# Kernel optimization log

Hardware: AMD Instinct MI355X
Metric: run time of the kernel (lower is better)

Reference implementation:

```python
import jax, jax.numpy as jnp
import numpy as np

N, C, H, W = 2, 256, 128, 128
NH, P = 8, 4
DH = C // NH
PAD = 1            # int(sqrt(n_points)//2)
HP, WP = H + 2 * PAD, W + 2 * PAD
LQ = H * W
DW_KS = 7


def _grid():
    # _generate_dilation_grids with n_points=4, dilation_rates=[1]:
    # kernel_size=2, linspace(0,1,2); torch stacks [y, x] (y-first quirk preserved)
    lin = np.linspace(0.0, 1.0, 2, dtype=np.float32)
    ky, kx = np.meshgrid(lin, lin, indexing='ij')
    return jnp.asarray(np.stack([ky, kx], -1).reshape(P, 2))  # (P, 2)


def _forward(query, reference_points, dw_kernel, dw_bias, ln_w, ln_b,
             W_off, b_off, W_attn, b_attn, W_val, b_val, W_out, b_out):
    # ---- dw_conv branch: depthwise 7x7 conv + channel LayerNorm + exact GELU ----
    q_img = query.transpose(0, 2, 1).reshape(N, C, H, W)
    q_img = jax.lax.conv_general_dilated(
        q_img, dw_kernel, (1, 1), [(3, 3), (3, 3)],
        dimension_numbers=('NCHW', 'OIHW', 'NCHW'), feature_group_count=C
    ) + dw_bias[None, :, None, None]
    mu = q_img.mean(axis=1, keepdims=True)
    var = ((q_img - mu) ** 2).mean(axis=1, keepdims=True)
    q_img = (q_img - mu) * jax.lax.rsqrt(var + 1e-5) * ln_w[None, :, None, None] + ln_b[None, :, None, None]
    q_img = jax.nn.gelu(q_img, approximate=False)
    q = q_img.transpose(0, 2, 3, 1).reshape(N, LQ, C)

    # ---- value projection + zero padding around the H x W map ----
    value = q @ W_val + b_val
    value = jnp.pad(value.reshape(N, H, W, C), ((0, 0), (PAD, PAD), (PAD, PAD), (0, 0)))
    v = value.reshape(N, HP * WP, NH, DH).transpose(0, 2, 1, 3)  # (N, NH, S, DH)

    # ---- offsets, sigmoid attention weights ----
    off = (q @ W_off + b_off).reshape(N, LQ, NH, 1, P, 2)
    attn = jax.nn.sigmoid(q @ W_attn + b_attn).reshape(N, LQ, NH, P)  # n_levels=1

    grid = _grid()[None, None, None, None, :, :]               # (1,1,1,1,P,2)
    norm = jnp.array([WP, HP], dtype=query.dtype)              # (W, H) normalizer
    loc = reference_points[:, :, None, :, None, :] + (grid + off) / norm
    loc = loc[:, :, :, 0, :, :]                                # (N, LQ, NH, P, 2)

    # grid_sample bilinear, align_corners=False, zero padding
    x = loc[..., 0] * WP - 0.5
    y = loc[..., 1] * HP - 0.5
    x0 = jnp.floor(x)
    y0 = jnp.floor(y)
    wx1 = x - x0
    wx0 = 1.0 - wx1
    wy1 = y - y0
    wy0 = 1.0 - wy1
    x0i = x0.astype(jnp.int32)
    y0i = y0.astype(jnp.int32)

    def gather(xi, yi):
        valid = (xi >= 0) & (xi < WP) & (yi >= 0) & (yi < HP)
        idx = jnp.clip(yi, 0, HP - 1) * WP + jnp.clip(xi, 0, WP - 1)
        idx = idx.transpose(0, 2, 1, 3).reshape(N, NH, LQ * P)
        g = jnp.take_along_axis(v, idx[..., None], axis=2)     # (N, NH, LQ*P, DH)
        m = valid.transpose(0, 2, 1, 3).reshape(N, NH, LQ * P, 1)
        return jnp.where(m, g, 0.0)

    def wmul(w):
        return w.transpose(0, 2, 1, 3).reshape(N, NH, LQ * P, 1)

    samp = (gather(x0i, y0i) * wmul(wx0 * wy0)
            + gather(x0i + 1, y0i) * wmul(wx1 * wy0)
            + gather(x0i, y0i + 1) * wmul(wx0 * wy1)
            + gather(x0i + 1, y0i + 1) * wmul(wx1 * wy1))      # (N, NH, LQ*P, DH)

    samp = samp.reshape(N, NH, LQ, P, DH)
    aw = attn.transpose(0, 2, 1, 3)[..., None]                 # (N, NH, LQ, P, 1)
    out = (samp * aw).sum(axis=3)                              # (N, NH, LQ, DH)
    out = out.transpose(0, 2, 1, 3).reshape(N, LQ, C)
    return out @ W_out + b_out


def setup_inputs() -> dict:
    key = jax.random.key(0)
    ks = jax.random.split(key, 8)
    return dict(
        query=jax.random.normal(ks[0], (N, LQ, C), jnp.float32),
        reference_points=jax.random.uniform(ks[1], (N, LQ, 1, 2), dtype=jnp.float32),
        input_spatial_shapes=jnp.array([[HP, WP]], dtype=jnp.int32),
        input_level_start_index=jnp.zeros((1,), dtype=jnp.int32),
        dw_kernel=jax.random.normal(ks[2], (C, 1, DW_KS, DW_KS), jnp.float32) * 0.05,
        dw_bias=jnp.zeros((C,), jnp.float32),
        ln_w=jnp.ones((C,), jnp.float32),
        ln_b=jnp.zeros((C,), jnp.float32),
        W_off=jax.random.normal(ks[3], (C, NH * P * 2), jnp.float32) * 0.01,
        b_off=jnp.zeros((NH * P * 2,), jnp.float32),
        W_attn=jax.random.normal(ks[4], (C, NH * P), jnp.float32) * 0.02,
        b_attn=jnp.zeros((NH * P,), jnp.float32),
        W_val=jax.random.normal(ks[5], (C, C), jnp.float32) * (1.0 / 16.0),
        b_val=jnp.zeros((C,), jnp.float32),
        W_out=jax.random.normal(ks[6], (C, C), jnp.float32) * (1.0 / 16.0),
        b_out=jnp.zeros((C,), jnp.float32),
    )


def reference(query, reference_points, input_spatial_shapes, input_level_start_index,
              dw_kernel, dw_bias, ln_w, ln_b, W_off, b_off, W_attn, b_attn,
              W_val, b_val, W_out, b_out):
    # input_spatial_shapes / input_level_start_index are static metadata (baked into constants)
    return _forward(query, reference_points, dw_kernel, dw_bias, ln_w, ln_b,
                    W_off, b_off, W_attn, b_attn, W_val, b_val, W_out, b_out)
```

## Files before the change

kernel.cpp:

```cpp
#include <hip/hip_runtime.h>
#include <hip/hip_bf16.h>
#include <hip/hip_fp16.h>
#include <math.h>

#define NB   2
#define CC   256
#define HH   128
#define WW   128
#define HPP  130
#define WPP  130
#define LQ   16384

typedef __attribute__((ext_vector_type(8))) short short8;
typedef __attribute__((ext_vector_type(8))) unsigned short u16x8;
typedef __attribute__((ext_vector_type(4))) float f32x4;
typedef __attribute__((ext_vector_type(4))) unsigned int u32x4;

static __device__ __forceinline__ unsigned short f2bf(float f) {
    __hip_bfloat16 h = __float2bfloat16(f);
    return __builtin_bit_cast(unsigned short, h);
}
static __device__ __forceinline__ float bf2f(unsigned short u) {
    unsigned int x = ((unsigned int)u) << 16;
    return __builtin_bit_cast(float, x);
}

static __device__ __forceinline__ float gelu_fast(float x) {
    float u = x * x;
    float t = x * fmaf(0.044715f, u, 1.0f);
    float e = __builtin_amdgcn_exp2f(t * 2.3022083f);
    float r = __builtin_amdgcn_rcpf(e + 1.0f);
    return x - x * r;
}

__global__ __launch_bounds__(256) void prep_kernel(
    const float* __restrict__ dwk,
    const float* __restrict__ Wval,
    const float* __restrict__ Wout,
    const float* __restrict__ Woff, const float* __restrict__ boff,
    const float* __restrict__ Wattn, const float* __restrict__ battn,
    const float* __restrict__ query,
    __half* __restrict__ kth,
    unsigned short* __restrict__ wt_val,
    unsigned short* __restrict__ wt_out,
    unsigned short* __restrict__ wt_oa,
    float* __restrict__ b_oa,
    unsigned short* __restrict__ vpad,
    __half* __restrict__ qh)
{
    int b = blockIdx.x;
    int t = threadIdx.x;
    if (b < 49) {
        kth[b * CC + t] = __float2half(dwk[t * 49 + b]);
    } else if (b < 305) {
        int k = b - 49;
        wt_val[(size_t)t * 256 + k] = f2bf(Wval[(size_t)k * 256 + t]);
    } else if (b < 561) {
        int k = b - 305;
        wt_out[(size_t)t * 256 + k] = f2bf(Wout[(size_t)k * 256 + t]);
    } else if (b < 817) {
        int k = b - 561;
        if (t < 128) {
            float v = 0.f, bb = 0.f;
            if (t < 64)      { v = Woff[(size_t)k * 64 + t];        bb = boff[t]; }
            else if (t < 96) { v = Wattn[(size_t)k * 32 + (t - 64)]; bb = battn[t - 64]; }
            wt_oa[(size_t)t * 256 + k] = f2bf(v);
            if (k == 0) b_oa[t] = bb;
        }
    } else if (b < 1849) {
        int bb = b - 817;
        int n = (bb >= 516) ? 1 : 0;
        int i = bb - n * 516;
        int y, x;
        if (i < 130)      { y = 0;           x = i; }
        else if (i < 260) { y = 129;         x = i - 130; }
        else if (i < 388) { y = i - 260 + 1; x = 0; }
        else              { y = i - 388 + 1; x = 129; }
        vpad[(((size_t)n * HPP + y) * WPP + x) * CC + t] = 0;
    } else {
        size_t idx0 = (size_t)(b - 1849) * 2048 + (size_t)t * 8;
        const float4* src = reinterpret_cast<const float4*>(query + idx0);
        float4 f0 = src[0];
        float4 f1 = src[1];
        __half2 h0 = __floats2half2_rn(f0.x, f0.y);
        __half2 h1 = __floats2half2_rn(f0.z, f0.w);
        __half2 h2 = __floats2half2_rn(f1.x, f1.y);
        __half2 h3 = __floats2half2_rn(f1.z, f1.w);
        u32x4 o;
        o.x = __builtin_bit_cast(unsigned int, h0);
        o.y = __builtin_bit_cast(unsigned int, h1);
        o.z = __builtin_bit_cast(unsigned int, h2);
        o.w = __builtin_bit_cast(unsigned int, h3);
        *reinterpret_cast<u32x4*>(qh + idx0) = o;
    }
}

__global__ __launch_bounds__(128) void conv_ln_gelu_kernel(
    const __half* __restrict__ qh,
    const __half* __restrict__ kth,
    const float* __restrict__ kbias,
    const float* __restrict__ lnw,
    const float* __restrict__ lnb,
    unsigned short* __restrict__ qact)
{
    int t  = threadIdx.x;
    int w0 = blockIdx.x * 8;
    int h  = blockIdx.y;
    int n  = blockIdx.z;

    const __half2* qn  = reinterpret_cast<const __half2*>(qh + (size_t)n * LQ * CC) + t;
    const __half2* ktc = reinterpret_cast<const __half2*>(kth) + t;

    __half2 acc[8];
    #pragma unroll
    for (int i = 0; i < 8; ++i) acc[i] = __half2(0.f, 0.f);

    if (w0 >= 8 && w0 <= 112 && h >= 3 && h <= 124) {
        #pragma unroll
        for (int ky = 0; ky < 7; ++ky) {
            const __half2* qrow = qn + ((size_t)(h + ky - 3) * WW + (w0 - 3)) * 128;
            __half2 wt[7];
            #pragma unroll
            for (int kx = 0; kx < 7; ++kx)
                wt[kx] = ktc[(ky * 7 + kx) * 128];
            __half2 in[14];
            #pragma unroll
            for (int j = 0; j < 14; ++j)
                in[j] = qrow[(size_t)j * 128];
            #pragma unroll
            for (int i = 0; i < 8; ++i)
                #pragma unroll
                for (int kx = 0; kx < 7; ++kx)
                    acc[i] = __hfma2(in[i + kx], wt[kx], acc[i]);
        }
    } else {
        #pragma unroll
        for (int ky = 0; ky < 7; ++ky) {
            int iy = h + ky - 3;
            if (iy < 0 || iy >= HH) continue;
            const __half2* qrow = qn + (size_t)iy * WW * 128;
            __half2 wt[7];
            #pragma unroll
            for (int kx = 0; kx < 7; ++kx)
                wt[kx] = ktc[(ky * 7 + kx) * 128];
            __half2 in[14];
            #pragma unroll
            for (int j = 0; j < 14; ++j) {
                int ix = w0 - 3 + j;
                in[j] = (ix >= 0 && ix < WW) ? qrow[(size_t)ix * 128]
                                             : __half2(0.f, 0.f);
            }
            #pragma unroll
            for (int i = 0; i < 8; ++i)
                #pragma unroll
                for (int kx = 0; kx < 7; ++kx)
                    acc[i] = __hfma2(in[i + kx], wt[kx], acc[i]);
        }
    }

    float b0 = kbias[2 * t];
    float b1 = kbias[2 * t + 1];
    float a0[8], a1[8];
    #pragma unroll
    for (int i = 0; i < 8; ++i) {
        a0[i] = __low2float(acc[i])  + b0;
        a1[i] = __high2float(acc[i]) + b1;
    }

    __shared__ float lsum[8][2];
    __shared__ float lsq[8][2];
    int lane = t & 63;
    int wv   = t >> 6;

    #pragma unroll
    for (int i = 0; i < 8; ++i) {
        float s  = a0[i] + a1[i];
        float sq = a0[i] * a0[i] + a1[i] * a1[i];
        #pragma unroll
        for (int m = 1; m < 64; m <<= 1) {
            s  += __shfl_xor(s,  m);
            sq += __shfl_xor(sq, m);
        }
        if (lane == 0) { lsum[i][wv] = s; lsq[i][wv] = sq; }
    }
    __syncthreads();

    float lw0 = lnw[2 * t], lw1 = lnw[2 * t + 1];
    float lb0 = lnb[2 * t], lb1 = lnb[2 * t + 1];
    unsigned short* qo = qact + (((size_t)n * LQ) + (size_t)h * WW + w0) * CC + 2 * t;

    #pragma unroll
    for (int i = 0; i < 8; ++i) {
        float s   = lsum[i][0] + lsum[i][1];
        float sq  = lsq[i][0]  + lsq[i][1];
        float mu  = s * (1.0f / 256.0f);
        float var = sq * (1.0f / 256.0f) - mu * mu;
        float inv = rsqrtf(var + 1e-5f);
        float g0 = gelu_fast((a0[i] - mu) * inv * lw0 + lb0);
        float g1 = gelu_fast((a1[i] - mu) * inv * lw1 + lb1);
        ushort2 o;
        o.x = f2bf(g0);
        o.y = f2bf(g1);
        *reinterpret_cast<ushort2*>(qo + (size_t)i * CC) = o;
    }
}

__global__ __launch_bounds__(256) void gemm_val_oa(
    const unsigned short* __restrict__ A,
    const unsigned short* __restrict__ Bv, const float* __restrict__ bv_,
    unsigned short* __restrict__ Cv,
    const unsigned short* __restrict__ Bo, const float* __restrict__ bo_,
    float* __restrict__ Co)
{
    __shared__ unsigned short Al[128][72];
    __shared__ unsigned short Bl[128][72];

    bool oam = (blockIdx.y == 2);
    const unsigned short* Bt = oam ? Bo : Bv;
    const float* bias = oam ? bo_ : bv_;
    int bn = oam ? 0 : blockIdx.y * 128;

    int t    = threadIdx.x;
    int bm   = blockIdx.x * 128;
    int wid  = t >> 6;
    int lane = t & 63;
    int wr   = wid >> 1;
    int wc   = wid & 1;
    int lr   = lane & 15;
    int lg   = lane >> 4;

    int srow = t >> 1;
    int sseg = (t & 1) << 5;

    const unsigned short* gA = A + (size_t)(bm + srow) * 256 + sseg;
    const unsigned short* gB = Bt + (size_t)(bn + srow) * 256 + sseg;
    unsigned short* lA = &Al[srow][sseg];
    unsigned short* lB = &Bl[srow][sseg];

    f32x4 acc[4][4] = {};

    for (int kt = 0; kt < 4; ++kt) {
        const unsigned short* ga = gA + kt * 64;
        const unsigned short* gb = gB + kt * 64;
        u32x4 a0 = *(const u32x4*)(ga);
        u32x4 a1 = *(const u32x4*)(ga + 8);
        u32x4 a2 = *(const u32x4*)(ga + 16);
        u32x4 a3 = *(const u32x4*)(ga + 24);
        u32x4 b0 = *(const u32x4*)(gb);
        u32x4 b1 = *(const u32x4*)(gb + 8);
        u32x4 b2 = *(const u32x4*)(gb + 16);
        u32x4 b3 = *(const u32x4*)(gb + 24);
        *(u32x4*)(lA)      = a0;
        *(u32x4*)(lA + 8)  = a1;
        *(u32x4*)(lA + 16) = a2;
        *(u32x4*)(lA + 24) = a3;
        *(u32x4*)(lB)      = b0;
        *(u32x4*)(lB + 8)  = b1;
        *(u32x4*)(lB + 16) = b2;
        *(u32x4*)(lB + 24) = b3;
        __syncthreads();

        #pragma unroll
        for (int kk = 0; kk < 2; ++kk) {
            short8 af[4], bfr[4];
            #pragma unroll
            for (int m = 0; m < 4; ++m)
                af[m] = *(const short8*)(&Al[wr * 64 + m * 16 + lr][kk * 32 + lg * 8]);
            #pragma unroll
            for (int nn = 0; nn < 4; ++nn)
                bfr[nn] = *(const short8*)(&Bl[wc * 64 + nn * 16 + lr][kk * 32 + lg * 8]);
            #pragma unroll
            for (int m = 0; m < 4; ++m)
                #pragma unroll
                for (int nn = 0; nn < 4; ++nn)
                    acc[m][nn] = __builtin_amdgcn_mfma_f32_16x16x32_bf16(
                        af[m], bfr[nn], acc[m][nn], 0, 0, 0);
        }
        __syncthreads();
    }

    float bvv[4];
    #pragma unroll
    for (int nn = 0; nn < 4; ++nn) bvv[nn] = bias[bn + wc * 64 + nn * 16 + lr];

    #pragma unroll
    for (int m = 0; m < 4; ++m) {
        #pragma unroll
        for (int j = 0; j < 4; ++j) {
            int row = bm + wr * 64 + m * 16 + lg * 4 + j;
            if (oam) {
                size_t rbase = (size_t)row * 128;
                #pragma unroll
                for (int nn = 0; nn < 4; ++nn) {
                    int col = wc * 64 + nn * 16 + lr;
                    Co[rbase + col] = acc[m][nn][j] + bvv[nn];
                }
            } else {
                int nb = row >> 14;
                int hw = row & 16383;
                int hh = hw >> 7;
                int ww = hw & 127;
                size_t rbase = (((size_t)nb * HPP + (hh + 1)) * WPP + (ww + 1)) * CC;
                #pragma unroll
                for (int nn = 0; nn < 4; ++nn) {
                    int col = bn + wc * 64 + nn * 16 + lr;
                    Cv[rbase + col] = f2bf(acc[m][nn][j] + bvv[nn]);
                }
            }
        }
    }
}

__global__ __launch_bounds__(256) void gemm_mfma_row(
    const unsigned short* __restrict__ A,
    const unsigned short* __restrict__ Bt,
    const float* __restrict__ bias,
    float* __restrict__ C,
    int Nn)
{
    __shared__ unsigned short Al[128][72];
    __shared__ unsigned short Bl[128][72];

    int t    = threadIdx.x;
    int bm   = blockIdx.x * 128;
    int bn   = blockIdx.y * 128;
    int wid  = t >> 6;
    int lane = t & 63;
    int wr   = wid >> 1;
    int wc   = wid & 1;
    int lr   = lane & 15;
    int lg   = lane >> 4;

    int srow = t >> 1;
    int sseg = (t & 1) << 5;

    const unsigned short* gA = A + (size_t)(bm + srow) * 256 + sseg;
    const unsigned short* gB = Bt + (size_t)(bn + srow) * 256 + sseg;
    unsigned short* lA = &Al[srow][sseg];
    unsigned short* lB = &Bl[srow][sseg];

    f32x4 acc[4][4] = {};

    for (int kt = 0; kt < 4; ++kt) {
        const unsigned short* ga = gA + kt * 64;
        const unsigned short* gb = gB + kt * 64;
        u32x4 a0 = *(const u32x4*)(ga);
        u32x4 a1 = *(const u32x4*)(ga + 8);
        u32x4 a2 = *(const u32x4*)(ga + 16);
        u32x4 a3 = *(const u32x4*)(ga + 24);
        u32x4 b0 = *(const u32x4*)(gb);
        u32x4 b1 = *(const u32x4*)(gb + 8);
        u32x4 b2 = *(const u32x4*)(gb + 16);
        u32x4 b3 = *(const u32x4*)(gb + 24);
        *(u32x4*)(lA)      = a0;
        *(u32x4*)(lA + 8)  = a1;
        *(u32x4*)(lA + 16) = a2;
        *(u32x4*)(lA + 24) = a3;
        *(u32x4*)(lB)      = b0;
        *(u32x4*)(lB + 8)  = b1;
        *(u32x4*)(lB + 16) = b2;
        *(u32x4*)(lB + 24) = b3;
        __syncthreads();

        #pragma unroll
        for (int kk = 0; kk < 2; ++kk) {
            short8 af[4], bfr[4];
            #pragma unroll
            for (int m = 0; m < 4; ++m)
                af[m] = *(const short8*)(&Al[wr * 64 + m * 16 + lr][kk * 32 + lg * 8]);
            #pragma unroll
            for (int nn = 0; nn < 4; ++nn)
                bfr[nn] = *(const short8*)(&Bl[wc * 64 + nn * 16 + lr][kk * 32 + lg * 8]);
            #pragma unroll
            for (int m = 0; m < 4; ++m)
                #pragma unroll
                for (int nn = 0; nn < 4; ++nn)
                    acc[m][nn] = __builtin_amdgcn_mfma_f32_16x16x32_bf16(
                        af[m], bfr[nn], acc[m][nn], 0, 0, 0);
        }
        __syncthreads();
    }

    float bvv[4];
    #pragma unroll
    for (int nn = 0; nn < 4; ++nn) bvv[nn] = bias[bn + wc * 64 + nn * 16 + lr];

    #pragma unroll
    for (int m = 0; m < 4; ++m) {
        #pragma unroll
        for (int j = 0; j < 4; ++j) {
            int row = bm + wr * 64 + m * 16 + lg * 4 + j;
            size_t rbase = (size_t)row * Nn;
            #pragma unroll
            for (int nn = 0; nn < 4; ++nn) {
                int col = bn + wc * 64 + nn * 16 + lr;
                C[rbase + col] = acc[m][nn][j] + bvv[nn];
            }
        }
    }
}

__global__ __launch_bounds__(256) void sampler_kernel(
    const float* __restrict__ rp,
    const float* __restrict__ oa,
    const unsigned short* __restrict__ vpad,
    unsigned short* __restrict__ outb)
{
    __shared__ int4   sIdx[8][4][8];
    __shared__ float4 sW[8][4][8];

    int tid  = threadIdx.x;
    int row0 = blockIdx.x * 8;

    {
        int rl   = tid >> 5;
        int hp   = tid & 31;
        int head = hp >> 2;
        int p    = hp & 3;
        int row  = row0 + rl;

        float ref0 = rp[(size_t)row * 2 + 0];
        float ref1 = rp[(size_t)row * 2 + 1];
        float o0 = oa[(size_t)row * 128 + head * 8 + p * 2 + 0];
        float o1 = oa[(size_t)row * 128 + head * 8 + p * 2 + 1];
        float al = oa[(size_t)row * 128 + 64 + head * 4 + p];
        float a  = 1.0f / (1.0f + __builtin_amdgcn_exp2f(-al * 1.4426950409f));

        float gy = (float)(p >> 1);
        float gx = (float)(p & 1);
        float x = ref0 * WPP + gy + o0 - 0.5f;
        float y = ref1 * HPP + gx + o1 - 0.5f;

        float x0f = floorf(x), y0f = floorf(y);
        int   x0  = (int)x0f,  y0  = (int)y0f;
        float wx1 = x - x0f, wx0 = 1.f - wx1;
        float wy1 = y - y0f, wy0 = 1.f - wy1;
        int x1 = x0 + 1, y1 = y0 + 1;

        bool vx0 = (x0 >= 0) & (x0 < WPP);
        bool vx1 = (x1 >= 0) & (x1 < WPP);
        bool vy0 = (y0 >= 0) & (y0 < HPP);
        bool vy1 = (y1 >= 0) & (y1 < HPP);
        int cx0 = min(max(x0, 0), WPP - 1);
        int cx1 = min(max(x1, 0), WPP - 1);
        int cy0 = min(max(y0, 0), HPP - 1);
        int cy1 = min(max(y1, 0), HPP - 1);

        int4 id;
        id.x = cy0 * WPP + cx0;
        id.y = cy0 * WPP + cx1;
        id.z = cy1 * WPP + cx0;
        id.w = cy1 * WPP + cx1;
        float4 w;
        w.x = (vx0 && vy0) ? a * wx0 * wy0 : 0.f;
        w.y = (vx1 && vy0) ? a * wx1 * wy0 : 0.f;
        w.z = (vx0 && vy1) ? a * wx0 * wy1 : 0.f;
        w.w = (vx1 && vy1) ? a * wx1 * wy1 : 0.f;

        sIdx[rl][p][head] = id;
        sW[rl][p][head]   = w;
    }
    __syncthreads();

    int rl   = tid >> 5;
    int c0   = (tid & 31) * 8;
    int head = (tid & 31) >> 2;
    int row  = row0 + rl;
    int n    = row >> 14;
    const unsigned short* vbase = vpad + (size_t)n * HPP * WPP * CC + c0;

    float acc[8] = {};
    #pragma unroll
    for (int p = 0; p < 4; ++p) {
        int4   id = sIdx[rl][p][head];
        float4 w  = sW[rl][p][head];
        u16x8 g0 = *reinterpret_cast<const u16x8*>(vbase + (size_t)id.x * CC);
        u16x8 g1 = *reinterpret_cast<const u16x8*>(vbase + (size_t)id.y * CC);
        u16x8 g2 = *reinterpret_cast<const u16x8*>(vbase + (size_t)id.z * CC);
        u16x8 g3 = *reinterpret_cast<const u16x8*>(vbase + (size_t)id.w * CC);
        #pragma unroll
        for (int j = 0; j < 8; ++j) {
            acc[j] += w.x * bf2f(g0[j]) + w.y * bf2f(g1[j])
                    + w.z * bf2f(g2[j]) + w.w * bf2f(g3[j]);
        }
    }
    u16x8 o;
    #pragma unroll
    for (int j = 0; j < 8; ++j) o[j] = f2bf(acc[j]);
    *reinterpret_cast<u16x8*>(&outb[(size_t)row * CC + c0]) = o;
}

extern "C" void kernel_launch(void* const* d_in, const int* in_sizes, int n_in,
                              void* d_out, int out_size, void* d_ws, size_t ws_size,
                              hipStream_t stream)
{
    const float* query = (const float*)d_in[0];
    const float* rp    = (const float*)d_in[1];
    const float* dwk   = (const float*)d_in[4];
    const float* dwb   = (const float*)d_in[5];
    const float* lnw   = (const float*)d_in[6];
    const float* lnb   = (const float*)d_in[7];
    const float* Woff  = (const float*)d_in[8];
    const float* boff  = (const float*)d_in[9];
    const float* Wattn = (const float*)d_in[10];
    const float* battn = (const float*)d_in[11];
    const float* Wval  = (const float*)d_in[12];
    const float* bval  = (const float*)d_in[13];
    const float* Wout  = (const float*)d_in[14];
    const float* bout  = (const float*)d_in[15];
    float* out = (float*)d_out;

    const int M = NB * LQ;

    uint8_t* w8 = (uint8_t*)d_ws;
    unsigned short* q_act  = (unsigned short*)w8;
    unsigned short* v_pad  = (unsigned short*)(w8 + 16777216);
    float*          oa     = (float*)(w8 + 34082816);
    __half*         qh     = (__half*)(w8 + 50860032);
    unsigned short* wt_val = (unsigned short*)(w8 + 67637248);
    unsigned short* wt_out = (unsigned short*)(w8 + 67768320);
    unsigned short* wt_oa  = (unsigned short*)(w8 + 67899392);
    float*          b_oa   = (float*)(w8 + 67964928);
    __half*         kth    = (__half*)(w8 + 67965440);
    unsigned short* out_attn = q_act;

    prep_kernel<<<5945, 256, 0, stream>>>(
        dwk, Wval, Wout, Woff, boff, Wattn, battn, query,
        kth, wt_val, wt_out, wt_oa, b_oa, v_pad, qh);

    {
        dim3 grid(WW / 8, HH, NB);
        conv_ln_gelu_kernel<<<grid, 128, 0, stream>>>(
            qh, kth, dwb, lnw, lnb, q_act);
    }

    {
        dim3 grid(M / 128, 3);
        gemm_val_oa<<<grid, 256, 0, stream>>>(
            q_act, wt_val, bval, v_pad, wt_oa, b_oa, oa);
    }

    sampler_kernel<<<M / 8, 256, 0, stream>>>(rp, oa, v_pad, out_attn);

    {
        dim3 grid(M / 128, 2);
        gemm_mfma_row<<<grid, 256, 0, stream>>>(out_attn, wt_out, bout, out, 256);
    }
}
```

Measured before the change: 84.74 us.

## Map full channel row to one wavefront in depthwise conv+LN+GELU kernel

Reworks the conv/LayerNorm/GELU kernel so each 64-lane wavefront handles all 256 channels of 8 pixels (4 channels per lane) instead of splitting channels across two wavefronts. The LayerNorm reduction then runs entirely through warp shuffles, with no shared memory or __syncthreads, and stores become 8-byte. Blocks now hold 4 wavefronts covering 32 pixels. Each lane keeps twice the accumulators and inputs, which raises register pressure and may lower occupancy. The per-lane half2 loads are now strided by 4 channels rather than contiguous.

```diff
diff --git a/kernel.cpp b/kernel.cpp
--- a/kernel.cpp
+++ b/kernel.cpp
@@ -95,7 +95,7 @@
     }
 }
 
-__global__ __launch_bounds__(128) void conv_ln_gelu_kernel(
+__global__ __launch_bounds__(256) void conv_ln_gelu_kernel(
     const __half* __restrict__ qh,
     const __half* __restrict__ kth,
     const float* __restrict__ kbias,
@@ -103,35 +103,46 @@
     const float* __restrict__ lnb,
     unsigned short* __restrict__ qact)
 {
-    int t  = threadIdx.x;
-    int w0 = blockIdx.x * 8;
-    int h  = blockIdx.y;
-    int n  = blockIdx.z;
-
-    const __half2* qn  = reinterpret_cast<const __half2*>(qh + (size_t)n * LQ * CC) + t;
-    const __half2* ktc = reinterpret_cast<const __half2*>(kth) + t;
-
-    __half2 acc[8];
-    #pragma unroll
-    for (int i = 0; i < 8; ++i) acc[i] = __half2(0.f, 0.f);
+    int lane = threadIdx.x & 63;
+    int wv   = threadIdx.x >> 6;
+    int w0   = blockIdx.x * 32 + wv * 8;
+    int h    = blockIdx.y;
+    int n    = blockIdx.z;
+    int c2   = lane * 2;
+
+    const __half2* qn  = reinterpret_cast<const __half2*>(qh) + (size_t)(n * LQ) * 128 + c2;
+    const __half2* ktc = reinterpret_cast<const __half2*>(kth) + c2;
+
+    __half2 acc0[8], acc1[8];
+    #pragma unroll
+    for (int i = 0; i < 8; ++i) {
+        acc0[i] = __half2(0.f, 0.f);
+        acc1[i] = __half2(0.f, 0.f);
+    }
 
     if (w0 >= 8 && w0 <= 112 && h >= 3 && h <= 124) {
         #pragma unroll
         for (int ky = 0; ky < 7; ++ky) {
             const __half2* qrow = qn + ((size_t)(h + ky - 3) * WW + (w0 - 3)) * 128;
-            __half2 wt[7];
-            #pragma unroll
-            for (int kx = 0; kx < 7; ++kx)
-                wt[kx] = ktc[(ky * 7 + kx) * 128];
-            __half2 in[14];
-            #pragma unroll
-            for (int j = 0; j < 14; ++j)
-                in[j] = qrow[(size_t)j * 128];
+            __half2 wta[7], wtb[7];
+            #pragma unroll
+            for (int kx = 0; kx < 7; ++kx) {
+                wta[kx] = ktc[(ky * 7 + kx) * 128];
+                wtb[kx] = ktc[(ky * 7 + kx) * 128 + 1];
+            }
+            __half2 ina[14], inb[14];
+            #pragma unroll
+            for (int j = 0; j < 14; ++j) {
+                ina[j] = qrow[(size_t)j * 128];
+                inb[j] = qrow[(size_t)j * 128 + 1];
+            }
             #pragma unroll
             for (int i = 0; i < 8; ++i)
                 #pragma unroll
-                for (int kx = 0; kx < 7; ++kx)
-                    acc[i] = __hfma2(in[i + kx], wt[kx], acc[i]);
+                for (int kx = 0; kx < 7; ++kx) {
+                    acc0[i] = __hfma2(ina[i + kx], wta[kx], acc0[i]);
+                    acc1[i] = __hfma2(inb[i + kx], wtb[kx], acc1[i]);
+                }
         }
     } else {
         #pragma unroll
@@ -139,69 +150,64 @@
             int iy = h + ky - 3;
             if (iy < 0 || iy >= HH) continue;
             const __half2* qrow = qn + (size_t)iy * WW * 128;
-            __half2 wt[7];
-            #pragma unroll
-            for (int kx = 0; kx < 7; ++kx)
-                wt[kx] = ktc[(ky * 7 + kx) * 128];
-            __half2 in[14];
+            __half2 wta[7], wtb[7];
+            #pragma unroll
+            for (int kx = 0; kx < 7; ++kx) {
+                wta[kx] = ktc[(ky * 7 + kx) * 128];
+                wtb[kx] = ktc[(ky * 7 + kx) * 128 + 1];
+            }
+            __half2 ina[14], inb[14];
             #pragma unroll
             for (int j = 0; j < 14; ++j) {
                 int ix = w0 - 3 + j;
-                in[j] = (ix >= 0 && ix < WW) ? qrow[(size_t)ix * 128]
-                                             : __half2(0.f, 0.f);
+                bool ok = (ix >= 0 && ix < WW);
+                ina[j] = ok ? qrow[(size_t)ix * 128]     : __half2(0.f, 0.f);
+                inb[j] = ok ? qrow[(size_t)ix * 128 + 1] : __half2(0.f, 0.f);
             }
             #pragma unroll
             for (int i = 0; i < 8; ++i)
                 #pragma unroll
-                for (int kx = 0; kx < 7; ++kx)
-                    acc[i] = __hfma2(in[i + kx], wt[kx], acc[i]);
-        }
-    }
-
-    float b0 = kbias[2 * t];
-    float b1 = kbias[2 * t + 1];
-    float a0[8], a1[8];
+                for (int kx = 0; kx < 7; ++kx) {
+                    acc0[i] = __hfma2(ina[i + kx], wta[kx], acc0[i]);
+                    acc1[i] = __hfma2(inb[i + kx], wtb[kx], acc1[i]);
+                }
+        }
+    }
+
+    int c4 = lane * 4;
+    float kb0 = kbias[c4], kb1 = kbias[c4 + 1], kb2 = kbias[c4 + 2], kb3 = kbias[c4 + 3];
+    float a[8][4];
     #pragma unroll
     for (int i = 0; i < 8; ++i) {
-        a0[i] = __low2float(acc[i])  + b0;
-        a1[i] = __high2float(acc[i]) + b1;
-    }
-
-    __shared__ float lsum[8][2];
-    __shared__ float lsq[8][2];
-    int lane = t & 63;
-    int wv   = t >> 6;
+        a[i][0] = __low2float(acc0[i])  + kb0;
+        a[i][1] = __high2float(acc0[i]) + kb1;
+        a[i][2] = __low2float(acc1[i])  + kb2;
+        a[i][3] = __high2float(acc1[i]) + kb3;
+    }
+
+    float lw0 = lnw[c4], lw1 = lnw[c4 + 1], lw2 = lnw[c4 + 2], lw3 = lnw[c4 + 3];
+    float lb0 = lnb[c4], lb1 = lnb[c4 + 1], lb2 = lnb[c4 + 2], lb3 = lnb[c4 + 3];
+    unsigned short* qo = qact + (((size_t)n * LQ) + (size_t)h * WW + w0) * CC + c4;
 
     #pragma unroll
     for (int i = 0; i < 8; ++i) {
-        float s  = a0[i] + a1[i];
-        float sq = a0[i] * a0[i] + a1[i] * a1[i];
+        float s  = a[i][0] + a[i][1] + a[i][2] + a[i][3];
+        float sq = a[i][0]*a[i][0] + a[i][1]*a[i][1]
+                 + a[i][2]*a[i][2] + a[i][3]*a[i][3];
         #pragma unroll
         for (int m = 1; m < 64; m <<= 1) {
             s  += __shfl_xor(s,  m);
             sq += __shfl_xor(sq, m);
         }
-        if (lane == 0) { lsum[i][wv] = s; lsq[i][wv] = sq; }
-    }
-    __syncthreads();
-
-    float lw0 = lnw[2 * t], lw1 = lnw[2 * t + 1];
-    float lb0 = lnb[2 * t], lb1 = lnb[2 * t + 1];
-    unsigned short* qo = qact + (((size_t)n * LQ) + (size_t)h * WW + w0) * CC + 2 * t;
-
-    #pragma unroll
-    for (int i = 0; i < 8; ++i) {
-        float s   = lsum[i][0] + lsum[i][1];
-        float sq  = lsq[i][0]  + lsq[i][1];
         float mu  = s * (1.0f / 256.0f);
         float var = sq * (1.0f / 256.0f) - mu * mu;
         float inv = rsqrtf(var + 1e-5f);
-        float g0 = gelu_fast((a0[i] - mu) * inv * lw0 + lb0);
-        float g1 = gelu_fast((a1[i] - mu) * inv * lw1 + lb1);
-        ushort2 o;
-        o.x = f2bf(g0);
-        o.y = f2bf(g1);
-        *reinterpret_cast<ushort2*>(qo + (size_t)i * CC) = o;
+        ushort4 o;
+        o.x = f2bf(gelu_fast((a[i][0] - mu) * inv * lw0 + lb0));
+        o.y = f2bf(gelu_fast((a[i][1] - mu) * inv * lw1 + lb1));
+        o.z = f2bf(gelu_fast((a[i][2] - mu) * inv * lw2 + lb2));
+        o.w = f2bf(gelu_fast((a[i][3] - mu) * inv * lw3 + lb3));
+        *reinterpret_cast<ushort4*>(qo + (size_t)i * CC) = o;
     }
 }
 
@@ -529,8 +535,8 @@
         kth, wt_val, wt_out, wt_oa, b_oa, v_pad, qh);
 
     {
-        dim3 grid(WW / 8, HH, NB);
-        conv_ln_gelu_kernel<<<grid, 128, 0, stream>>>(
+        dim3 grid(WW / 32, HH, NB);
+        conv_ln_gelu_kernel<<<grid, 256, 0, stream>>>(
             qh, kth, dwb, lnw, lnb, q_act);
     }
 
```

After: 86.63 us. 1.02x slower.
